# Kernel tuning notes

Hardware: AMD Instinct MI355X
Metric: run time of the kernel (lower is better)

## Reference

```python
import jax, jax.numpy as jnp
import numpy as np

N_NODES = 50000
N_EDGES = 600000
F_IN = 57
HID = 128
NEG_SLOPE = 0.2  # PyG GATConv default leaky_relu slope


def setup_inputs() -> dict:
    key = jax.random.key(0)
    ks = jax.random.split(key, 10)
    s = lambda k, shape, fan: jax.random.normal(k, shape, jnp.float32) / np.float32(np.sqrt(fan))
    x = jax.random.normal(ks[0], (N_NODES, F_IN), jnp.float32)
    edge_index = jax.random.randint(ks[1], (2, N_EDGES), 0, N_NODES)
    return {
        "x": x,
        "edge_index": edge_index,
        # layer1: GATConv(57 -> 128, heads=1)
        "W_gat": s(ks[2], (F_IN, HID), F_IN),
        "a_src": s(ks[3], (HID,), HID),
        "a_dst": s(ks[4], (HID,), HID),
        "b_gat": jnp.zeros((HID,), jnp.float32),
        # layer2: SAGEConv(128 -> 128, aggr='mean'): lin_l (with bias) on aggregated, lin_r (no bias) on self
        "W_l": s(ks[5], (HID, HID), HID),
        "b_l": jnp.zeros((HID,), jnp.float32),
        "W_r": s(ks[6], (HID, HID), HID),
        # layer3: Linear(128 -> 1)
        "W_out": s(ks[7], (HID, 1), HID),
        "b_out": jnp.zeros((1,), jnp.float32),
    }


def _gat_conv(x, src, dst, W, a_s, a_d, b, n):
    # PyG GATConv (heads=1): adds self-loops, attention softmax over incoming edges per dst node.
    loop = jnp.arange(n)
    src = jnp.concatenate([src, loop])
    dst = jnp.concatenate([dst, loop])
    h = x @ W                                   # [N, H]
    logit = jax.nn.leaky_relu((h @ a_s)[src] + (h @ a_d)[dst], NEG_SLOPE)  # [E+N]
    lmax = jax.lax.stop_gradient(jax.ops.segment_max(logit, dst, num_segments=n))
    ex = jnp.exp(logit - lmax[dst])
    denom = jax.ops.segment_sum(ex, dst, num_segments=n)
    alpha = ex / denom[dst]
    out = jax.ops.segment_sum(alpha[:, None] * h[src], dst, num_segments=n)  # [N, H]
    return out + b


def _sage_conv_mean(x, src, dst, W_l, b_l, W_r, n):
    # PyG SAGEConv: out = lin_l(mean_{j->i} x_j) + lin_r(x_i); no self-loops.
    msum = jax.ops.segment_sum(x[src], dst, num_segments=n)          # [N, H]
    cnt = jax.ops.segment_sum(jnp.ones_like(src, jnp.float32), dst, num_segments=n)
    mean = msum / jnp.maximum(cnt, 1.0)[:, None]
    return mean @ W_l + b_l + x @ W_r


def reference(x, edge_index, W_gat, a_src, a_dst, b_gat, W_l, b_l, W_r, W_out, b_out):
    n = x.shape[0]
    src, dst = edge_index[0], edge_index[1]
    h = jax.nn.relu(_gat_conv(x, src, dst, W_gat, a_src, a_dst, b_gat, n))
    h = jax.nn.relu(_sage_conv_mean(h, src, dst, W_l, b_l, W_r, n))
    return jax.nn.sigmoid(h @ W_out + b_out)  # [N, 1]
```

## Files before the change

### kernel.cpp

```cpp
#include <hip/hip_runtime.h>

#define NN 50000
#define NE 600000
#define F_IN 57
#define HID 128
#define NEG 0.2f
#define NB_SCAN ((NN + 255) / 256)

#define GIN_NODES 64
#define NB_GIN ((NN + GIN_NODES - 1) / GIN_NODES)
#define XST 68

#define DN_NODES 64
#define NB_DENSE ((NN + DN_NODES - 1) / DN_NODES)

typedef unsigned short bf16_t;
typedef __attribute__((ext_vector_type(8))) short bf16x8;
typedef __attribute__((ext_vector_type(4))) float f32x4;

__device__ __forceinline__ float leaky(float v) { return v >= 0.f ? v : NEG * v; }
__device__ __forceinline__ float bf2f(bf16_t u) { return __uint_as_float(((unsigned)u) << 16); }
__device__ __forceinline__ bf16_t f2bf(float f) {
    unsigned u = __float_as_uint(f);
    return (bf16_t)((u + 0x7FFFu + ((u >> 16) & 1u)) >> 16);
}

__global__ __launch_bounds__(256) void k_gat_in(
    const float* __restrict__ x, const float* __restrict__ Wg,
    const float* __restrict__ a_s, const float* __restrict__ a_d,
    bf16_t* __restrict__ h, float* __restrict__ hs, float* __restrict__ hd) {
    __shared__ float WgS[F_IN * HID];
    __shared__ float xsT[F_IN][XST];
    int tid = threadIdx.x;
    int node0 = blockIdx.x * GIN_NODES;
    {
        const float4* g = (const float4*)Wg;
        float4* s = (float4*)WgS;
        for (int i = tid; i < F_IN * HID / 4; i += 256) s[i] = g[i];
    }
    for (int i = tid; i < GIN_NODES * F_IN; i += 256) {
        int n = i / F_IN;
        int k = i - n * F_IN;
        int gn = node0 + n;
        if (gn >= NN) gn = NN - 1;
        xsT[k][n] = x[gn * F_IN + k];
    }
    __syncthreads();

    int fq = tid & 31, nq = tid >> 5;
    int f0 = fq * 4, nb = nq * 8;
    float acc[8][4];
#pragma unroll
    for (int i = 0; i < 8; ++i)
#pragma unroll
        for (int j = 0; j < 4; ++j) acc[i][j] = 0.f;

    for (int k = 0; k < F_IN; ++k) {
        float4 w = *(const float4*)&WgS[k * HID + f0];
        float4 xa = *(const float4*)&xsT[k][nb];
        float4 xb = *(const float4*)&xsT[k][nb + 4];
        float xv[8] = {xa.x, xa.y, xa.z, xa.w, xb.x, xb.y, xb.z, xb.w};
        float wv[4] = {w.x, w.y, w.z, w.w};
#pragma unroll
        for (int i = 0; i < 8; ++i)
#pragma unroll
            for (int j = 0; j < 4; ++j)
                acc[i][j] = fmaf(xv[i], wv[j], acc[i][j]);
    }

    float4 as4 = *(const float4*)(a_s + f0);
    float4 ad4 = *(const float4*)(a_d + f0);
    float ps[8], pd[8];
#pragma unroll
    for (int i = 0; i < 8; ++i) {
        int gn = node0 + nb + i;
        if (gn < NN) {
            ushort4 hv;
            hv.x = f2bf(acc[i][0]); hv.y = f2bf(acc[i][1]);
            hv.z = f2bf(acc[i][2]); hv.w = f2bf(acc[i][3]);
            *(ushort4*)(h + (size_t)gn * HID + f0) = hv;
        }
        ps[i] = acc[i][0] * as4.x + acc[i][1] * as4.y + acc[i][2] * as4.z + acc[i][3] * as4.w;
        pd[i] = acc[i][0] * ad4.x + acc[i][1] * ad4.y + acc[i][2] * ad4.z + acc[i][3] * ad4.w;
    }
#pragma unroll
    for (int off = 16; off > 0; off >>= 1) {
#pragma unroll
        for (int i = 0; i < 8; ++i) {
            ps[i] += __shfl_xor(ps[i], off);
            pd[i] += __shfl_xor(pd[i], off);
        }
    }
    if (fq == 0) {
#pragma unroll
        for (int i = 0; i < 8; ++i) {
            int gn = node0 + nb + i;
            if (gn < NN) { hs[gn] = ps[i]; hd[gn] = pd[i]; }
        }
    }
}

__global__ __launch_bounds__(256) void k_pack_w(
    const float* __restrict__ Wl, const float* __restrict__ Wr,
    bf16_t* __restrict__ Bp, int* __restrict__ deg) {
    if (blockIdx.x >= 16) {
        int idx4 = (blockIdx.x - 16) * 256 + threadIdx.x;
        if (idx4 < NN / 4 + 1) {
            int i = idx4 * 4;
            if (i + 4 <= NN) *(int4*)(deg + i) = (int4){0, 0, 0, 0};
            else for (; i < NN; ++i) deg[i] = 0;
        }
        return;
    }
    int idx = blockIdx.x * 256 + threadIdx.x;
    if (idx >= 8 * 8 * 64) return;
    int lane = idx & 63;
    int kb = (idx >> 6) & 7;
    int nt = idx >> 9;
    int col = nt * 16 + (lane & 15);
    int kbase = kb * 32 + (lane >> 4) * 8;
    bf16_t v[8];
#pragma unroll
    for (int j = 0; j < 8; ++j) {
        int k = kbase + j;
        float w = (k < HID) ? Wl[k * HID + col] : Wr[(k - HID) * HID + col];
        v[j] = f2bf(w);
    }
    ushort4* o = (ushort4*)(Bp + (size_t)idx * 8);
    ushort4 lo, hi;
    lo.x = v[0]; lo.y = v[1]; lo.z = v[2]; lo.w = v[3];
    hi.x = v[4]; hi.y = v[5]; hi.z = v[6]; hi.w = v[7];
    o[0] = lo; o[1] = hi;
}

__global__ void k_hist(const int* __restrict__ dst, int* __restrict__ deg) {
    int e = blockIdx.x * blockDim.x + threadIdx.x;
    if (e < NE) atomicAdd(&deg[dst[e]], 1);
}

__global__ void k_scan1(const int* __restrict__ deg, int* __restrict__ rptr, int* __restrict__ bsum) {
    int t = threadIdx.x;
    int i = blockIdx.x * 256 + t;
    int v = (i < NN) ? deg[i] : 0;
    __shared__ int s[256];
    s[t] = v;
    __syncthreads();
    for (int off = 1; off < 256; off <<= 1) {
        int x = (t >= off) ? s[t - off] : 0;
        __syncthreads();
        s[t] += x;
        __syncthreads();
    }
    if (i < NN) rptr[i] = s[t] - v;
    if (t == 255) bsum[blockIdx.x] = s[255];
}

__global__ void k_scan3(int* __restrict__ rptr, const int* __restrict__ bsum,
                        int* __restrict__ wptr) {
    int t = threadIdx.x;
    int v = (t < NB_SCAN && t < blockIdx.x) ? bsum[t] : 0;
#pragma unroll
    for (int off = 32; off > 0; off >>= 1) v += __shfl_xor(v, off);
    __shared__ int wsum[4];
    if ((t & 63) == 0) wsum[t >> 6] = v;
    __syncthreads();
    int pre = wsum[0] + wsum[1] + wsum[2] + wsum[3];
    int i = blockIdx.x * 256 + t;
    if (i < NN) {
        int r = rptr[i] + pre;
        rptr[i] = r;
        wptr[i] = r;
    }
}

__global__ void k_fill(const int* __restrict__ src, const int* __restrict__ dst,
                       int* __restrict__ wptr, int* __restrict__ esrc) {
    int e = blockIdx.x * blockDim.x + threadIdx.x;
    if (e >= NE) return;
    int d = dst[e];
    int pos = atomicAdd(&wptr[d], 1);
    esrc[pos] = src[e];
}

__global__ __launch_bounds__(256) void k_gat_agg(
    const int* __restrict__ rptr, const int* __restrict__ deg,
    const int* __restrict__ esrc, const float* __restrict__ hs,
    const float* __restrict__ hd, const bf16_t* __restrict__ h,
    const float* __restrict__ bg, bf16_t* __restrict__ h1) {
    int tid = threadIdx.x;
    int row = blockIdx.x * 4 + (tid >> 6);
    if (row >= NN) return;
    int lane = tid & 63;
    int slot = lane >> 4;
    int f8 = lane & 15;

    int start = rptr[row];
    int dn = deg[row];
    int end = start + dn;
    float hdr = hd[row];
    float wself = __expf(leaky(hs[row] + hdr));

    float a[8];
#pragma unroll
    for (int j = 0; j < 8; ++j) a[j] = 0.f;
    float denL = 0.f;

    if (slot == 0) {
        bf16x8 r = *(const bf16x8*)(h + (size_t)row * HID + f8 * 8);
#pragma unroll
        for (int j = 0; j < 8; ++j) a[j] = wself * bf2f((bf16_t)r[j]);
    }

    int e = start;
    for (; e + 8 <= end; e += 8) {
        int s0 = esrc[e + slot];
        int s1 = esrc[e + 4 + slot];
        float w0 = __expf(leaky(hs[s0] + hdr));
        float w1 = __expf(leaky(hs[s1] + hdr));
        bf16x8 r0 = *(const bf16x8*)(h + (size_t)s0 * HID + f8 * 8);
        bf16x8 r1 = *(const bf16x8*)(h + (size_t)s1 * HID + f8 * 8);
        denL += w0 + w1;
#pragma unroll
        for (int j = 0; j < 8; ++j) {
            a[j] = fmaf(w0, bf2f((bf16_t)r0[j]), a[j]);
            a[j] = fmaf(w1, bf2f((bf16_t)r1[j]), a[j]);
        }
    }
    for (; e < end; e += 4) {
        int i = e + slot;
        bool act = i < end;
        int sn = esrc[act ? i : end - 1];
        float w = act ? __expf(leaky(hs[sn] + hdr)) : 0.f;
        bf16x8 r = *(const bf16x8*)(h + (size_t)sn * HID + f8 * 8);
        denL += w;
#pragma unroll
        for (int j = 0; j < 8; ++j) a[j] = fmaf(w, bf2f((bf16_t)r[j]), a[j]);
    }

#pragma unroll
    for (int j = 0; j < 8; ++j) {
        a[j] += __shfl_xor(a[j], 16);
        a[j] += __shfl_xor(a[j], 32);
    }
    denL += __shfl_xor(denL, 16);
    denL += __shfl_xor(denL, 32);
    float inv = 1.f / (wself + denL);

    if (lane < 16) {
        float4 b0 = *(const float4*)(bg + lane * 8);
        float4 b1 = *(const float4*)(bg + lane * 8 + 4);
        float bb[8] = {b0.x, b0.y, b0.z, b0.w, b1.x, b1.y, b1.z, b1.w};
        bf16x8 o;
#pragma unroll
        for (int j = 0; j < 8; ++j) {
            float v = a[j] * inv + bb[j];
            o[j] = (short)f2bf(v > 0.f ? v : 0.f);
        }
        *(bf16x8*)(h1 + (size_t)row * HID + lane * 8) = o;
    }
}

__global__ __launch_bounds__(256) void k_sage_gather(
    const int* __restrict__ rptr, const int* __restrict__ deg,
    const int* __restrict__ esrc, const bf16_t* __restrict__ h1,
    bf16_t* __restrict__ mean) {
    int tid = threadIdx.x;
    int row = blockIdx.x * 4 + (tid >> 6);
    if (row >= NN) return;
    int lane = tid & 63;
    int slot = lane >> 4;
    int f8 = lane & 15;

    int start = rptr[row];
    int dn = deg[row];
    int end = start + dn;

    float a[8];
#pragma unroll
    for (int j = 0; j < 8; ++j) a[j] = 0.f;

    int e = start;
    for (; e + 8 <= end; e += 8) {
        int s0 = esrc[e + slot];
        int s1 = esrc[e + 4 + slot];
        bf16x8 r0 = *(const bf16x8*)(h1 + (size_t)s0 * HID + f8 * 8);
        bf16x8 r1 = *(const bf16x8*)(h1 + (size_t)s1 * HID + f8 * 8);
#pragma unroll
        for (int j = 0; j < 8; ++j)
            a[j] += bf2f((bf16_t)r0[j]) + bf2f((bf16_t)r1[j]);
    }
    for (; e < end; e += 4) {
        int i = e + slot;
        bool act = i < end;
        int sn = esrc[act ? i : end - 1];
        bf16x8 r = *(const bf16x8*)(h1 + (size_t)sn * HID + f8 * 8);
        float w = act ? 1.f : 0.f;
#pragma unroll
        for (int j = 0; j < 8; ++j) a[j] = fmaf(w, bf2f((bf16_t)r[j]), a[j]);
    }

#pragma unroll
    for (int j = 0; j < 8; ++j) {
        a[j] += __shfl_xor(a[j], 16);
        a[j] += __shfl_xor(a[j], 32);
    }
    if (lane < 16) {
        float inv = 1.f / (float)(dn > 0 ? dn : 1);
        bf16x8 o;
#pragma unroll
        for (int j = 0; j < 8; ++j) o[j] = (short)f2bf(a[j] * inv);
        *(bf16x8*)(mean + (size_t)row * HID + lane * 8) = o;
    }
}

__global__ __launch_bounds__(256) void k_dense_mfma(
    const bf16_t* __restrict__ mean, const bf16_t* __restrict__ h1,
    const bf16_t* __restrict__ Bp, const float* __restrict__ bl,
    const float* __restrict__ Wout, const float* __restrict__ bout,
    float* __restrict__ out) {
    int tid = threadIdx.x;
    int lane = tid & 63;
    int wv = tid >> 6;
    int node0 = blockIdx.x * DN_NODES + wv * 16;
    int arow = lane & 15;
    int kg = lane >> 4;
    int gn = node0 + arow;
    if (gn >= NN) gn = NN - 1;
    const bf16_t* mrow = mean + (size_t)gn * HID;
    const bf16_t* srow = h1 + (size_t)gn * HID;
    const bf16x8* bp = (const bf16x8*)Bp;

    f32x4 acc[8];
#pragma unroll
    for (int n = 0; n < 8; ++n) acc[n] = (f32x4){0.f, 0.f, 0.f, 0.f};

#pragma unroll
    for (int kb = 0; kb < 8; ++kb) {
        int k0 = kb * 32 + kg * 8;
        bf16x8 a = (kb < 4) ? *(const bf16x8*)(mrow + k0)
                            : *(const bf16x8*)(srow + (k0 - HID));
#pragma unroll
        for (int n = 0; n < 8; ++n) {
            bf16x8 b = bp[((n * 8 + kb) << 6) + lane];
            acc[n] = __builtin_amdgcn_mfma_f32_16x16x32_bf16(a, b, acc[n], 0, 0, 0);
        }
    }

    float pr[4] = {0.f, 0.f, 0.f, 0.f};
#pragma unroll
    for (int n = 0; n < 8; ++n) {
        int f = n * 16 + arow;
        float b = bl[f];
        float wo = Wout[f];
#pragma unroll
        for (int r = 0; r < 4; ++r) {
            float v = fmaxf(acc[n][r] + b, 0.f);
            pr[r] = fmaf(v, wo, pr[r]);
        }
    }
#pragma unroll
    for (int off = 8; off > 0; off >>= 1) {
#pragma unroll
        for (int r = 0; r < 4; ++r) pr[r] += __shfl_xor(pr[r], off);
    }
    if (arow == 0) {
        float bo = bout[0];
#pragma unroll
        for (int r = 0; r < 4; ++r) {
            int gno = node0 + kg * 4 + r;
            if (gno < NN) out[gno] = 1.f / (1.f + __expf(-(pr[r] + bo)));
        }
    }
}

extern "C" void kernel_launch(void* const* d_in, const int* in_sizes, int n_in,
                              void* d_out, int out_size, void* d_ws, size_t ws_size,
                              hipStream_t stream) {
    const float* x    = (const float*)d_in[0];
    const int*   ei   = (const int*)d_in[1];
    const float* Wg   = (const float*)d_in[2];
    const float* a_s  = (const float*)d_in[3];
    const float* a_d  = (const float*)d_in[4];
    const float* bg   = (const float*)d_in[5];
    const float* Wl   = (const float*)d_in[6];
    const float* bl   = (const float*)d_in[7];
    const float* Wr   = (const float*)d_in[8];
    const float* Wout = (const float*)d_in[9];
    const float* bout = (const float*)d_in[10];
    float* out = (float*)d_out;

    const int* src = ei;
    const int* dst = ei + NE;

    bf16_t* h    = (bf16_t*)d_ws;
    bf16_t* h1   = h + (size_t)NN * HID;
    bf16_t* mean = h1 + (size_t)NN * HID;
    bf16_t* Bp   = mean + (size_t)NN * HID;
    float* hs = (float*)(Bp + 8 * 8 * 64 * 8);
    float* hd = hs + NN;
    int* deg  = (int*)(hd + NN);
    int* wptr = deg + NN;
    int* rptr = wptr + NN;
    int* bsum = rptr + NN;
    int* esrc = bsum + NB_SCAN;

    k_pack_w<<<16 + (NN / 4 + 255) / 256, 256, 0, stream>>>(Wl, Wr, Bp, deg);
    k_gat_in<<<NB_GIN, 256, 0, stream>>>(x, Wg, a_s, a_d, h, hs, hd);

    k_hist<<<(NE + 255) / 256, 256, 0, stream>>>(dst, deg);
    k_scan1<<<NB_SCAN, 256, 0, stream>>>(deg, rptr, bsum);
    k_scan3<<<NB_SCAN, 256, 0, stream>>>(rptr, bsum, wptr);
    k_fill<<<(NE + 255) / 256, 256, 0, stream>>>(src, dst, wptr, esrc);

    k_gat_agg<<<(NN + 3) / 4, 256, 0, stream>>>(rptr, deg, esrc, hs, hd, h, bg, h1);
    k_sage_gather<<<(NN + 3) / 4, 256, 0, stream>>>(rptr, deg, esrc, h1, mean);
    k_dense_mfma<<<NB_DENSE, 256, 0, stream>>>(mean, h1, Bp, bl, Wout, bout, out);
}
```

Baseline: 172.5 us.

## Merge front kernels and fuse CSR build into one cooperative kernel

Folds weight packing and degree zeroing into the GAT input projection kernel as extra blocks. It also replaces the separate histogram, two scan passes and fill kernels with one cooperative kernel that uses grid-wide syncs between phases. The aim is to cut kernel launch count and inter-kernel gaps. In exchange it relies on cooperative launch with 1024 resident blocks, and grid.sync adds its own barrier cost.

```diff
diff --git a/kernel.cpp b/kernel.cpp
--- a/kernel.cpp
+++ b/kernel.cpp
@@ -1,4 +1,7 @@
 #include <hip/hip_runtime.h>
+#include <hip/hip_cooperative_groups.h>
+
+namespace cg = cooperative_groups;
 
 #define NN 50000
 #define NE 600000
@@ -10,6 +13,10 @@
 #define GIN_NODES 64
 #define NB_GIN ((NN + GIN_NODES - 1) / GIN_NODES)
 #define XST 68
+#define NB_PACK 16
+#define NB_ZERO ((NN / 4 + 255) / 256)
+
+#define CSR_BLOCKS 1024
 
 #define DN_NODES 64
 #define NB_DENSE ((NN + DN_NODES - 1) / DN_NODES)
@@ -25,13 +32,44 @@
     return (bf16_t)((u + 0x7FFFu + ((u >> 16) & 1u)) >> 16);
 }
 
-__global__ __launch_bounds__(256) void k_gat_in(
+__global__ __launch_bounds__(256) void k_front(
     const float* __restrict__ x, const float* __restrict__ Wg,
     const float* __restrict__ a_s, const float* __restrict__ a_d,
-    bf16_t* __restrict__ h, float* __restrict__ hs, float* __restrict__ hd) {
+    const float* __restrict__ Wl, const float* __restrict__ Wr,
+    bf16_t* __restrict__ h, float* __restrict__ hs, float* __restrict__ hd,
+    bf16_t* __restrict__ Bp, int* __restrict__ deg) {
+    int tid = threadIdx.x;
+
+    if (blockIdx.x >= NB_GIN + NB_PACK) {
+        int idx4 = (blockIdx.x - NB_GIN - NB_PACK) * 256 + tid;
+        if (idx4 * 4 < NN) *(int4*)(deg + idx4 * 4) = (int4){0, 0, 0, 0};
+        return;
+    }
+    if (blockIdx.x >= NB_GIN) {
+        int idx = (blockIdx.x - NB_GIN) * 256 + tid;
+        if (idx >= 8 * 8 * 64) return;
+        int lane = idx & 63;
+        int kb = (idx >> 6) & 7;
+        int nt = idx >> 9;
+        int col = nt * 16 + (lane & 15);
+        int kbase = kb * 32 + (lane >> 4) * 8;
+        bf16_t v[8];
+#pragma unroll
+        for (int j = 0; j < 8; ++j) {
+            int k = kbase + j;
+            float w = (k < HID) ? Wl[k * HID + col] : Wr[(k - HID) * HID + col];
+            v[j] = f2bf(w);
+        }
+        ushort4* o = (ushort4*)(Bp + (size_t)idx * 8);
+        ushort4 lo, hi;
+        lo.x = v[0]; lo.y = v[1]; lo.z = v[2]; lo.w = v[3];
+        hi.x = v[4]; hi.y = v[5]; hi.z = v[6]; hi.w = v[7];
+        o[0] = lo; o[1] = hi;
+        return;
+    }
+
     __shared__ float WgS[F_IN * HID];
     __shared__ float xsT[F_IN][XST];
-    int tid = threadIdx.x;
     int node0 = blockIdx.x * GIN_NODES;
     {
         const float4* g = (const float4*)Wg;
@@ -100,86 +138,59 @@
     }
 }
 
-__global__ __launch_bounds__(256) void k_pack_w(
-    const float* __restrict__ Wl, const float* __restrict__ Wr,
-    bf16_t* __restrict__ Bp, int* __restrict__ deg) {
-    if (blockIdx.x >= 16) {
-        int idx4 = (blockIdx.x - 16) * 256 + threadIdx.x;
-        if (idx4 < NN / 4 + 1) {
-            int i = idx4 * 4;
-            if (i + 4 <= NN) *(int4*)(deg + i) = (int4){0, 0, 0, 0};
-            else for (; i < NN; ++i) deg[i] = 0;
-        }
-        return;
-    }
-    int idx = blockIdx.x * 256 + threadIdx.x;
-    if (idx >= 8 * 8 * 64) return;
-    int lane = idx & 63;
-    int kb = (idx >> 6) & 7;
-    int nt = idx >> 9;
-    int col = nt * 16 + (lane & 15);
-    int kbase = kb * 32 + (lane >> 4) * 8;
-    bf16_t v[8];
-#pragma unroll
-    for (int j = 0; j < 8; ++j) {
-        int k = kbase + j;
-        float w = (k < HID) ? Wl[k * HID + col] : Wr[(k - HID) * HID + col];
-        v[j] = f2bf(w);
-    }
-    ushort4* o = (ushort4*)(Bp + (size_t)idx * 8);
-    ushort4 lo, hi;
-    lo.x = v[0]; lo.y = v[1]; lo.z = v[2]; lo.w = v[3];
-    hi.x = v[4]; hi.y = v[5]; hi.z = v[6]; hi.w = v[7];
-    o[0] = lo; o[1] = hi;
-}
-
-__global__ void k_hist(const int* __restrict__ dst, int* __restrict__ deg) {
-    int e = blockIdx.x * blockDim.x + threadIdx.x;
-    if (e < NE) atomicAdd(&deg[dst[e]], 1);
-}
-
-__global__ void k_scan1(const int* __restrict__ deg, int* __restrict__ rptr, int* __restrict__ bsum) {
-    int t = threadIdx.x;
-    int i = blockIdx.x * 256 + t;
-    int v = (i < NN) ? deg[i] : 0;
+__global__ __launch_bounds__(256) void k_csr(
+    const int* __restrict__ src, const int* __restrict__ dst,
+    int* __restrict__ deg, int* __restrict__ rptr, int* __restrict__ wptr,
+    int* __restrict__ bsum, int* __restrict__ esrc) {
+    cg::grid_group grid = cg::this_grid();
+    int tid = threadIdx.x;
+    int gid = blockIdx.x * 256 + tid;
+    int gsz = gridDim.x * 256;
     __shared__ int s[256];
-    s[t] = v;
-    __syncthreads();
-    for (int off = 1; off < 256; off <<= 1) {
-        int x = (t >= off) ? s[t - off] : 0;
+    __shared__ int wsum[4];
+
+    for (int e = gid; e < NE; e += gsz) atomicAdd(&deg[dst[e]], 1);
+    grid.sync();
+
+    for (int tile = blockIdx.x; tile < NB_SCAN; tile += gridDim.x) {
+        int i = tile * 256 + tid;
+        int v = (i < NN) ? deg[i] : 0;
+        s[tid] = v;
         __syncthreads();
-        s[t] += x;
+        for (int off = 1; off < 256; off <<= 1) {
+            int xv = (tid >= off) ? s[tid - off] : 0;
+            __syncthreads();
+            s[tid] += xv;
+            __syncthreads();
+        }
+        if (i < NN) rptr[i] = s[tid] - v;
+        if (tid == 255) bsum[tile] = s[255];
         __syncthreads();
     }
-    if (i < NN) rptr[i] = s[t] - v;
-    if (t == 255) bsum[blockIdx.x] = s[255];
-}
-
-__global__ void k_scan3(int* __restrict__ rptr, const int* __restrict__ bsum,
-                        int* __restrict__ wptr) {
-    int t = threadIdx.x;
-    int v = (t < NB_SCAN && t < blockIdx.x) ? bsum[t] : 0;
-#pragma unroll
-    for (int off = 32; off > 0; off >>= 1) v += __shfl_xor(v, off);
-    __shared__ int wsum[4];
-    if ((t & 63) == 0) wsum[t >> 6] = v;
-    __syncthreads();
-    int pre = wsum[0] + wsum[1] + wsum[2] + wsum[3];
-    int i = blockIdx.x * 256 + t;
-    if (i < NN) {
-        int r = rptr[i] + pre;
-        rptr[i] = r;
-        wptr[i] = r;
-    }
-}
-
-__global__ void k_fill(const int* __restrict__ src, const int* __restrict__ dst,
-                       int* __restrict__ wptr, int* __restrict__ esrc) {
-    int e = blockIdx.x * blockDim.x + threadIdx.x;
-    if (e >= NE) return;
-    int d = dst[e];
-    int pos = atomicAdd(&wptr[d], 1);
-    esrc[pos] = src[e];
+    grid.sync();
+
+    for (int tile = blockIdx.x; tile < NB_SCAN; tile += gridDim.x) {
+        int v = (tid < NB_SCAN && tid < tile) ? bsum[tid] : 0;
+#pragma unroll
+        for (int off = 32; off > 0; off >>= 1) v += __shfl_xor(v, off);
+        if ((tid & 63) == 0) wsum[tid >> 6] = v;
+        __syncthreads();
+        int pre = wsum[0] + wsum[1] + wsum[2] + wsum[3];
+        int i = tile * 256 + tid;
+        if (i < NN) {
+            int r = rptr[i] + pre;
+            rptr[i] = r;
+            wptr[i] = r;
+        }
+        __syncthreads();
+    }
+    grid.sync();
+
+    for (int e = gid; e < NE; e += gsz) {
+        int d = dst[e];
+        int pos = atomicAdd(&wptr[d], 1);
+        esrc[pos] = src[e];
+    }
 }
 
 __global__ __launch_bounds__(256) void k_gat_agg(
@@ -404,13 +415,15 @@
     int* bsum = rptr + NN;
     int* esrc = bsum + NB_SCAN;
 
-    k_pack_w<<<16 + (NN / 4 + 255) / 256, 256, 0, stream>>>(Wl, Wr, Bp, deg);
-    k_gat_in<<<NB_GIN, 256, 0, stream>>>(x, Wg, a_s, a_d, h, hs, hd);
-
-    k_hist<<<(NE + 255) / 256, 256, 0, stream>>>(dst, deg);
-    k_scan1<<<NB_SCAN, 256, 0, stream>>>(deg, rptr, bsum);
-    k_scan3<<<NB_SCAN, 256, 0, stream>>>(rptr, bsum, wptr);
-    k_fill<<<(NE + 255) / 256, 256, 0, stream>>>(src, dst, wptr, esrc);
+    k_front<<<NB_GIN + NB_PACK + NB_ZERO, 256, 0, stream>>>(
+        x, Wg, a_s, a_d, Wl, Wr, h, hs, hd, Bp, deg);
+
+    {
+        void* args[] = {(void*)&src, (void*)&dst, (void*)&deg, (void*)&rptr,
+                        (void*)&wptr, (void*)&bsum, (void*)&esrc};
+        hipLaunchCooperativeKernel((void*)k_csr, dim3(CSR_BLOCKS), dim3(256),
+                                   args, 0, stream);
+    }
 
     k_gat_agg<<<(NN + 3) / 4, 256, 0, stream>>>(rptr, deg, esrc, hs, hd, h, bg, h1);
     k_sage_gather<<<(NN + 3) / 4, 256, 0, stream>>>(rptr, deg, esrc, h1, mean);
```

Result: slower. 453.8 us (+163.1%).
